# Performance work log

Hardware: AMD Instinct MI355X
Metric: run time of the kernel (lower is better)

## Reference

```python
import jax, jax.numpy as jnp
import numpy as np

B, S, D, H, W = 4, 9, 256, 32, 32
RATIO = 2
NH = 16
DK = D // NH            # 16 (module recomputes d_k = d_in // n_head)
HP, WP = H // RATIO, W // RATIO
QL = H * W              # 1024 query tokens
KL = S * HP * WP        # 2304 key/value tokens


def setup_inputs() -> dict:
    key = jax.random.key(0)
    ks = jax.random.split(key, 8)
    s = 0.02
    return {
        "x": jax.random.normal(ks[0], (B, S, D, H, W), jnp.float32),
        "conv_w": jax.random.normal(ks[1], (D, D, RATIO, RATIO), jnp.float32) * s,
        "conv_b": jnp.zeros((D,), jnp.float32),
        "gn_g": jnp.ones((D,), jnp.float32),
        "gn_b": jnp.zeros((D,), jnp.float32),
        "wq": jax.random.normal(ks[2], (D, NH * DK), jnp.float32) * s,
        "bq": jnp.zeros((NH * DK,), jnp.float32),
        "wkv": jax.random.normal(ks[3], (D, 2 * NH * DK), jnp.float32) * s,
        "bkv": jnp.zeros((2 * NH * DK,), jnp.float32),
        "pos_bias": jax.random.normal(ks[4], (NH, QL, KL), jnp.float32) * s,
        "proj_w": jax.random.normal(ks[5], (D, D), jnp.float32) * s,
        "proj_b": jnp.zeros((D,), jnp.float32),
    }


def reference(x, conv_w, conv_b, gn_g, gn_b, wq, bq, wkv, bkv, pos_bias, proj_w, proj_b):
    b, s, d, h, w = x.shape
    hp, wp = h // RATIO, w // RATIO

    # query stream: center frame, flattened -> (b, h*w, d)
    v_self = x[:, 4].reshape(b, d, h * w).transpose(0, 2, 1)

    # key/value stream: Conv2d(k=stride=ratio) + GroupNorm(NH groups) over all frames
    vn = x.reshape(b * s, d, h, w)
    vn = jax.lax.conv_general_dilated(
        vn, conv_w, window_strides=(RATIO, RATIO), padding="VALID",
        dimension_numbers=("NCHW", "OIHW", "NCHW"))
    vn = vn + conv_b[None, :, None, None]
    g = vn.reshape(b * s, NH, d // NH, hp, wp)
    mu = g.mean(axis=(2, 3, 4), keepdims=True)
    var = g.var(axis=(2, 3, 4), keepdims=True)
    g = (g - mu) * jax.lax.rsqrt(var + 1e-5)
    vn = g.reshape(b * s, d, hp, wp) * gn_g[None, :, None, None] + gn_b[None, :, None, None]
    # (b, s*hp*wp, d)
    vn = vn.reshape(b, s, d, hp, wp).transpose(0, 1, 3, 4, 2).reshape(b, s * hp * wp, d)

    # projections
    q = (v_self @ wq + bq).reshape(b, h * w, NH, DK)            # (b, Q, H, dk)
    kv = (vn @ wkv + bkv).reshape(b, -1, 2, NH, DK)             # (b, K, 2, H, dk)
    k, v = kv[:, :, 0], kv[:, :, 1]                             # (b, K, H, dk)

    # cross-attention with learned positional bias added to QK^T
    dots = jnp.einsum("bqhd,bkhd->hbqk", q, k) * (DK ** -0.5)
    dots = dots + pos_bias[:, None]                             # (H, b, Q, K)
    attn = jax.nn.softmax(dots, axis=-1)
    out = jnp.einsum("hbqk,bkhd->bqhd", attn, v)                # (b, Q, H, dk)
    out = out.reshape(b, h, w, NH * DK)                         # (n c) head-major
    out = out @ proj_w + proj_b                                 # (b, h, w, d)

    # SpatialVit: 'b h w c -> b c h w'
    return out.transpose(0, 3, 1, 2)
```

## Files before the change

### kernel.cpp

```cpp
#include <hip/hip_runtime.h>

#define NBATCH 4
#define NSEQ   9
#define ND     256
#define NHEAD  16
#define NDKv   16
#define NQ     1024
#define NKL    2304
#define NKLH   1152
#define NSAMP  36

constexpr long OFF_CONV = 0;
constexpr long OFF_VN   = 2359296;
constexpr long OFF_WT   = 3538944;
constexpr long OFF_Q    = 4718592;
constexpr long OFF_K    = 5242880;
constexpr long OFF_VT   = 6422528;
constexpr long OFF_AO   = 0;
constexpr long OFF_PN   = 1048576;
constexpr long OFF_PL   = 3145728;

using bf16x8 = __attribute__((ext_vector_type(8))) short;
using f32x4  = __attribute__((ext_vector_type(4))) float;

__device__ __forceinline__ float bf2f(unsigned short h) {
    unsigned int u = ((unsigned int)h) << 16;
    float f; __builtin_memcpy(&f, &u, 4); return f;
}
__device__ __forceinline__ unsigned short f2bf(float f) {
    unsigned int u; __builtin_memcpy(&u, &f, 4);
    u += 0x7fffu + ((u >> 16) & 1u);
    return (unsigned short)(u >> 16);
}
template<bool BF> __device__ __forceinline__ float ld1(const void* p, long i) {
    if constexpr (BF) return bf2f(((const unsigned short*)p)[i]);
    else return ((const float*)p)[i];
}
template<bool BF> __device__ __forceinline__ float4 ld4(const void* p, long i) {
    if constexpr (BF) { ushort4 v = *(const ushort4*)((const unsigned short*)p + i);
                        return make_float4(bf2f(v.x), bf2f(v.y), bf2f(v.z), bf2f(v.w)); }
    else return *(const float4*)((const float*)p + i);
}
template<bool BF> __device__ __forceinline__ void st1(void* p, long i, float v) {
    if constexpr (BF) ((unsigned short*)p)[i] = f2bf(v);
    else ((float*)p)[i] = v;
}
__device__ __forceinline__ bool detect_bf16(const void* gn_g) {
    return (*(const unsigned int*)gn_g) != 0x3F800000u;
}

template<bool BF>
__device__ void conv_body(const void* __restrict__ x, const void* __restrict__ cw,
                          const void* __restrict__ cb, float* __restrict__ ws) {
    __shared__ short lA[64 * 40];
    __shared__ short lB[128 * 40];
    const int tid  = threadIdx.x;
    const int n    = blockIdx.x;
    const int pq   = blockIdx.y;
    const int och  = blockIdx.z;
    const int wave = tid >> 6, lane = tid & 63;
    const int col  = lane & 15, quad = lane >> 4;

    f32x4 acc[4][2];
    #pragma unroll
    for (int mt = 0; mt < 4; ++mt)
        #pragma unroll
        for (int nt = 0; nt < 2; ++nt) acc[mt][nt] = {0.f, 0.f, 0.f, 0.f};

    const int icl  = tid >> 5;
    const int t5   = tid & 31;
    const int ihl  = t5 >> 2;
    const int iwg  = (t5 & 3) * 8;
    const int k0x  = icl * 4 + (ihl & 1) * 2;
    const int posx = (ihl >> 1) * 16 + (iwg >> 1);
    const long xrow = ((long)n * ND * 32 + (long)(pq * 8 + ihl)) * 32 + iwg;

    const int ocw = tid >> 3;
    const int kkw = (tid & 7) * 4;

    for (int kc = 0; kc < 32; ++kc) {
        __syncthreads();
        {
            const long xa = xrow + (long)(kc * 8 + icl) * 1024;
            float4 v0 = ld4<BF>(x, xa);
            float4 v1 = ld4<BF>(x, xa + 4);
            unsigned short us[8] = {f2bf(v0.x), f2bf(v0.y), f2bf(v0.z), f2bf(v0.w),
                                    f2bf(v1.x), f2bf(v1.y), f2bf(v1.z), f2bf(v1.w)};
            #pragma unroll
            for (int o = 0; o < 4; ++o)
                *(ushort2*)&lA[(posx + o) * 40 + k0x] = make_ushort2(us[2*o], us[2*o+1]);
        }
        #pragma unroll
        for (int j = 0; j < 4; ++j) {
            const int oc = ocw + j * 32;
            float4 wv = ld4<BF>(cw, (long)(och * 128 + oc) * 1024 + kc * 32 + kkw);
            unsigned int lo = (unsigned int)f2bf(wv.x) | ((unsigned int)f2bf(wv.y) << 16);
            unsigned int hi = (unsigned int)f2bf(wv.z) | ((unsigned int)f2bf(wv.w) << 16);
            *(uint2*)&lB[oc * 40 + kkw] = make_uint2(lo, hi);
        }
        __syncthreads();
        bf16x8 af[4];
        #pragma unroll
        for (int mt = 0; mt < 4; ++mt)
            af[mt] = *(const bf16x8*)&lA[(mt * 16 + col) * 40 + quad * 8];
        #pragma unroll
        for (int nt = 0; nt < 2; ++nt) {
            bf16x8 bfg = *(const bf16x8*)&lB[((wave * 2 + nt) * 16 + col) * 40 + quad * 8];
            #pragma unroll
            for (int mt = 0; mt < 4; ++mt)
                acc[mt][nt] = __builtin_amdgcn_mfma_f32_16x16x32_bf16(af[mt], bfg, acc[mt][nt], 0, 0, 0);
        }
    }

    float* co = ws + OFF_CONV + (long)n * 65536;
    #pragma unroll
    for (int nt = 0; nt < 2; ++nt) {
        const int oc = och * 128 + (wave * 2 + nt) * 16 + col;
        const float cbv = ld1<BF>(cb, oc);
        #pragma unroll
        for (int mt = 0; mt < 4; ++mt)
            #pragma unroll
            for (int r = 0; r < 4; ++r) {
                const int pos = pq * 64 + mt * 16 + quad * 4 + r;
                co[(long)pos * 256 + oc] = acc[mt][nt][r] + cbv;
            }
    }
}
__global__ void __launch_bounds__(256)
conv_k(const void* x, const void* cw, const void* cb, const void* gg, float* ws) {
    if (detect_bf16(gg)) conv_body<true>(x, cw, cb, ws);
    else                 conv_body<false>(x, cw, cb, ws);
}

template<bool BF>
__device__ void gn_body(const void* __restrict__ gn_g, const void* __restrict__ gn_b,
                        float* __restrict__ ws) {
    const int t = threadIdx.x;
    const int n = blockIdx.x;
    const int g = blockIdx.y;
    const float* row = ws + OFF_CONV + ((long)n * 256 + t) * 256 + g * 16;

    float v[16]; float s1 = 0.f, s2 = 0.f;
    #pragma unroll
    for (int q4 = 0; q4 < 4; ++q4) {
        float4 a = *(const float4*)(row + q4 * 4);
        v[q4*4+0] = a.x; v[q4*4+1] = a.y; v[q4*4+2] = a.z; v[q4*4+3] = a.w;
        s1 += (a.x + a.y) + (a.z + a.w);
        s2 += (a.x*a.x + a.y*a.y) + (a.z*a.z + a.w*a.w);
    }
    __shared__ float r1[4], r2[4];
    #pragma unroll
    for (int off = 32; off > 0; off >>= 1) {
        s1 += __shfl_down(s1, off, 64);
        s2 += __shfl_down(s2, off, 64);
    }
    if ((t & 63) == 0) { r1[t >> 6] = s1; r2[t >> 6] = s2; }
    __syncthreads();
    const float ts1 = r1[0] + r1[1] + r1[2] + r1[3];
    const float ts2 = r2[0] + r2[1] + r2[2] + r2[3];
    const float mean = ts1 * (1.0f / 4096.0f);
    const float var  = ts2 * (1.0f / 4096.0f) - mean * mean;
    const float inv  = rsqrtf(var + 1e-5f);

    const int b = n / NSEQ, s = n % NSEQ;
    float o[16];
    #pragma unroll
    for (int cl = 0; cl < 16; ++cl) {
        float gg = ld1<BF>(gn_g, g * 16 + cl);
        float bb = ld1<BF>(gn_b, g * 16 + cl);
        o[cl] = (v[cl] - mean) * inv * gg + bb;
    }
    unsigned short* dst = (unsigned short*)(ws + OFF_VN)
                          + ((long)b * NKL + s * 256 + t) * ND + g * 16;
    bf16x8 w0, w1;
    #pragma unroll
    for (int cl = 0; cl < 8; ++cl) {
        w0[cl] = (short)f2bf(o[cl]);
        w1[cl] = (short)f2bf(o[cl + 8]);
    }
    *(bf16x8*)dst       = w0;
    *(bf16x8*)(dst + 8) = w1;
}
__global__ void gn_k(const void* gg, const void* gb, float* ws) {
    if (detect_bf16(gg)) gn_body<true>(gg, gb, ws);
    else                 gn_body<false>(gg, gb, ws);
}

template<bool BF>
__device__ void tw_body(const void* __restrict__ wkv, float* __restrict__ ws) {
    __shared__ float tile[16][17];
    const int t = threadIdx.x;
    const int oc0 = blockIdx.x * 16;
    const int r = t >> 4, c = t & 15;
    unsigned short* wt = (unsigned short*)(ws + OFF_WT);
    for (int k0 = 0; k0 < ND; k0 += 16) {
        const float v = ld1<BF>(wkv, (long)(k0 + r) * 512 + oc0 + c);
        __syncthreads();
        tile[r][c] = v;
        __syncthreads();
        wt[(long)(oc0 + r) * ND + k0 + c] = f2bf(tile[c][r]);
    }
}
__global__ void __launch_bounds__(256)
tw_k(const void* wkv, const void* gg, float* ws) {
    if (detect_bf16(gg)) tw_body<true>(wkv, ws);
    else                 tw_body<false>(wkv, ws);
}

template<bool BF>
__device__ void q_body(const void* __restrict__ x, const void* __restrict__ wq,
                       const void* __restrict__ bq, float* __restrict__ ws) {
    const int lane = threadIdx.x;
    const int mb = blockIdx.x;
    const int ob = blockIdx.y;
    const int b  = mb >> 6;
    const int q0 = (mb & 63) * 16;
    const int oc = ob * 64 + lane;

    float acc[16];
    const float bqv = ld1<BF>(bq, oc);
    #pragma unroll
    for (int i = 0; i < 16; ++i) acc[i] = bqv;

    const long xoff = ((long)(b * NSEQ + 4) * ND) * NQ;
    for (int d = 0; d < ND; ++d) {
        const float wv = ld1<BF>(wq, (long)d * 256 + oc);
        const long vb = xoff + (long)d * NQ + q0;
        float4 a0 = ld4<BF>(x, vb + 0);
        float4 a1 = ld4<BF>(x, vb + 4);
        float4 a2 = ld4<BF>(x, vb + 8);
        float4 a3 = ld4<BF>(x, vb + 12);
        acc[0]  += a0.x * wv; acc[1]  += a0.y * wv; acc[2]  += a0.z * wv; acc[3]  += a0.w * wv;
        acc[4]  += a1.x * wv; acc[5]  += a1.y * wv; acc[6]  += a1.z * wv; acc[7]  += a1.w * wv;
        acc[8]  += a2.x * wv; acc[9]  += a2.y * wv; acc[10] += a2.z * wv; acc[11] += a2.w * wv;
        acc[12] += a3.x * wv; acc[13] += a3.y * wv; acc[14] += a3.z * wv; acc[15] += a3.w * wv;
    }
    const int h = oc >> 4, dk = oc & 15;
    unsigned short* qb = (unsigned short*)(ws + OFF_Q);
    #pragma unroll
    for (int i = 0; i < 16; ++i)
        qb[(((long)b * NHEAD + h) * NQ + q0 + i) * NDKv + dk] = f2bf(acc[i]);
}
__global__ void __launch_bounds__(64, 4)
q_k(const void* x, const void* wq, const void* bq, const void* gg, float* ws) {
    if (detect_bf16(gg)) q_body<true>(x, wq, bq, ws);
    else                 q_body<false>(x, wq, bq, ws);
}

template<bool BF>
__device__ void kv_body(const void* __restrict__ bkv, float* __restrict__ ws) {
    __shared__ short lA[64 * 32];
    __shared__ short lB[128 * 32];
    const int tid = threadIdx.x;
    const int b   = blockIdx.x / 36;
    const int t0  = (blockIdx.x % 36) * 64;
    const int ob  = blockIdx.y;
    const int wave = tid >> 6, lane = tid & 63;
    const int col = lane & 15, quad = lane >> 4;

    const unsigned short* vnb = (const unsigned short*)(ws + OFF_VN) + ((long)b * NKL + t0) * ND;
    const unsigned short* wtb = (const unsigned short*)(ws + OFF_WT) + (long)ob * 128 * ND;

    const int rS = tid >> 2;
    const int sS = (tid & 3) * 8;

    f32x4 acc[4][2];
    #pragma unroll
    for (int mt = 0; mt < 4; ++mt)
        #pragma unroll
        for (int nt = 0; nt < 2; ++nt) acc[mt][nt] = {0.f, 0.f, 0.f, 0.f};

    for (int kc = 0; kc < 8; ++kc) {
        __syncthreads();
        *(bf16x8*)&lA[rS * 32 + sS] =
            *(const bf16x8*)(vnb + (long)rS * ND + kc * 32 + sS);
        *(bf16x8*)&lB[rS * 32 + sS] =
            *(const bf16x8*)(wtb + (long)rS * ND + kc * 32 + sS);
        *(bf16x8*)&lB[(64 + rS) * 32 + sS] =
            *(const bf16x8*)(wtb + (long)(64 + rS) * ND + kc * 32 + sS);
        __syncthreads();
        bf16x8 af[4];
        #pragma unroll
        for (int mt = 0; mt < 4; ++mt)
            af[mt] = *(const bf16x8*)&lA[(mt * 16 + col) * 32 + quad * 8];
        #pragma unroll
        for (int nt = 0; nt < 2; ++nt) {
            bf16x8 bfg = *(const bf16x8*)&lB[((wave * 2 + nt) * 16 + col) * 32 + quad * 8];
            #pragma unroll
            for (int mt = 0; mt < 4; ++mt)
                acc[mt][nt] = __builtin_amdgcn_mfma_f32_16x16x32_bf16(af[mt], bfg, acc[mt][nt], 0, 0, 0);
        }
    }

    const bool isv = (ob >= 2);
    unsigned short* k16  = (unsigned short*)(ws + OFF_K);
    unsigned short* vt16 = (unsigned short*)(ws + OFF_VT);
    #pragma unroll
    for (int nt = 0; nt < 2; ++nt) {
        const int ocl = (wave * 2 + nt) * 16 + col;
        const int oc  = ob * 128 + ocl;
        const float bv = ld1<BF>(bkv, oc);
        const int oc2 = oc & 255, h = oc2 >> 4, dk = oc2 & 15;
        if (!isv) {
            #pragma unroll
            for (int mt = 0; mt < 4; ++mt)
                #pragma unroll
                for (int r = 0; r < 4; ++r) {
                    const int tok = t0 + mt * 16 + quad * 4 + r;
                    k16[((long)(b * NHEAD + h) * NKL + tok) * NDKv + dk] = f2bf(acc[mt][nt][r] + bv);
                }
        } else {
            #pragma unroll
            for (int mt = 0; mt < 4; ++mt) {
                const int tok = t0 + mt * 16 + quad * 4;
                ushort4 pk;
                pk.x = f2bf(acc[mt][nt][0] + bv);
                pk.y = f2bf(acc[mt][nt][1] + bv);
                pk.z = f2bf(acc[mt][nt][2] + bv);
                pk.w = f2bf(acc[mt][nt][3] + bv);
                *(ushort4*)&vt16[((long)(b * NHEAD + h) * 16 + dk) * NKL + tok] = pk;
            }
        }
    }
}
__global__ void __launch_bounds__(256)
kv_k(const void* bkv, const void* gg, float* ws) {
    if (detect_bf16(gg)) kv_body<true>(bkv, ws);
    else                 kv_body<false>(bkv, ws);
}

template<bool BF>
__device__ void attn_body(const void* __restrict__ pos_bias, float* __restrict__ ws) {
    __shared__ short lds[4 * 16 * 40];
    const int tid  = threadIdx.x;
    const int b    = tid >> 6;
    const int lane = tid & 63;
    const int qt   = blockIdx.x;
    const int h    = blockIdx.y;
    const int half = blockIdx.z;
    const int t0   = half * NKLH;
    const int bh = b * NHEAD + h;
    const int col  = lane & 15;
    const int quad = lane >> 4;
    short* myl = &lds[b * 640];

    const unsigned short* Qb = (const unsigned short*)(ws + OFF_Q);
    const unsigned short* Kb = (const unsigned short*)(ws + OFF_K);
    const unsigned short* Vt = (const unsigned short*)(ws + OFF_VT);

    bf16x8 qfrag = {0,0,0,0,0,0,0,0};
    if (quad < 2)
        qfrag = *(const bf16x8*)(Qb + (((long)bh * NQ + qt * 16 + col) * 16 + quad * 8));

    const unsigned short* Krows = Kb + ((long)bh * NKL + t0) * 16 + (long)col * 16 + (quad & 1) * 8;
    const unsigned short* Vrow  = Vt + ((long)bh * 16 + col) * NKL + t0 + quad * 8;
    const long pbase = ((long)h * NQ + qt * 16 + col) * NKL + t0 + quad * 4;

    f32x4 oacc = {0.f, 0.f, 0.f, 0.f};
    const f32x4 zc = {0.f, 0.f, 0.f, 0.f};
    float lsum = 0.f;

    auto do_chunk = [&](bf16x8 ck0, bf16x8 ck1, bf16x8 cv, float4 cb0, float4 cb1) {
        f32x4 s0 = __builtin_amdgcn_mfma_f32_16x16x32_bf16(ck0, qfrag, zc, 0, 0, 0);
        f32x4 s1 = __builtin_amdgcn_mfma_f32_16x16x32_bf16(ck1, qfrag, zc, 0, 0, 0);
        float p0 = __expf(s0[0] * 0.25f + cb0.x);
        float p1 = __expf(s0[1] * 0.25f + cb0.y);
        float p2 = __expf(s0[2] * 0.25f + cb0.z);
        float p3 = __expf(s0[3] * 0.25f + cb0.w);
        float r0 = __expf(s1[0] * 0.25f + cb1.x);
        float r1 = __expf(s1[1] * 0.25f + cb1.y);
        float r2 = __expf(s1[2] * 0.25f + cb1.z);
        float r3 = __expf(s1[3] * 0.25f + cb1.w);
        lsum += ((p0 + p1) + (p2 + p3)) + ((r0 + r1) + (r2 + r3));
        unsigned int lo0 = (unsigned int)f2bf(p0) | ((unsigned int)f2bf(p1) << 16);
        unsigned int hi0 = (unsigned int)f2bf(p2) | ((unsigned int)f2bf(p3) << 16);
        unsigned int lo1 = (unsigned int)f2bf(r0) | ((unsigned int)f2bf(r1) << 16);
        unsigned int hi1 = (unsigned int)f2bf(r2) | ((unsigned int)f2bf(r3) << 16);
        *(uint2*)(&myl[col * 40 + quad * 4])      = make_uint2(lo0, hi0);
        *(uint2*)(&myl[col * 40 + 16 + quad * 4]) = make_uint2(lo1, hi1);
        bf16x8 pfrag = *(const bf16x8*)(&myl[col * 40 + quad * 8]);
        oacc = __builtin_amdgcn_mfma_f32_16x16x32_bf16(pfrag, cv, oacc, 0, 0, 0);
    };

    bf16x8 kf0 = *(const bf16x8*)(Krows);
    bf16x8 kf1 = *(const bf16x8*)(Krows + 16L * 16);
    bf16x8 vf  = *(const bf16x8*)(Vrow);
    float4 pbA0 = ld4<BF>(pos_bias, pbase);
    float4 pbA1 = ld4<BF>(pos_bias, pbase + 16);
    float4 pbB0 = ld4<BF>(pos_bias, pbase + 32);
    float4 pbB1 = ld4<BF>(pos_bias, pbase + 48);

    for (int kb = 0; kb < NKLH; kb += 64) {
        {
            const bf16x8 ck0 = kf0, ck1 = kf1, cv = vf;
            const float4 cb0 = pbA0, cb1 = pbA1;
            const int nk = kb + 32;
            kf0 = *(const bf16x8*)(Krows + (long)nk * 16);
            kf1 = *(const bf16x8*)(Krows + (long)(nk + 16) * 16);
            vf  = *(const bf16x8*)(Vrow + nk);
            const int pk = (kb + 64 < NKLH) ? kb + 64 : 0;
            pbA0 = ld4<BF>(pos_bias, pbase + pk);
            pbA1 = ld4<BF>(pos_bias, pbase + pk + 16);
            do_chunk(ck0, ck1, cv, cb0, cb1);
        }
        {
            const bf16x8 ck0 = kf0, ck1 = kf1, cv = vf;
            const float4 cb0 = pbB0, cb1 = pbB1;
            const int nk = (kb + 64 < NKLH) ? kb + 64 : 0;
            kf0 = *(const bf16x8*)(Krows + (long)nk * 16);
            kf1 = *(const bf16x8*)(Krows + (long)(nk + 16) * 16);
            vf  = *(const bf16x8*)(Vrow + nk);
            const int pk = (kb + 96 < NKLH) ? kb + 96 : 0;
            pbB0 = ld4<BF>(pos_bias, pbase + pk);
            pbB1 = ld4<BF>(pos_bias, pbase + pk + 16);
            do_chunk(ck0, ck1, cv, cb0, cb1);
        }
    }

    lsum += __shfl_xor(lsum, 16, 64);
    lsum += __shfl_xor(lsum, 32, 64);

    float* pn = ws + OFF_PN + ((((long)half * NBATCH + b) * NHEAD + h) * NQ + qt * 16) * 16;
    #pragma unroll
    for (int r = 0; r < 4; ++r)
        pn[(long)(quad * 4 + r) * 16 + col] = oacc[r];
    if (quad == 0) {
        float* pl = ws + OFF_PL + (((long)half * NBATCH + b) * NHEAD + h) * NQ + qt * 16;
        pl[col] = lsum;
    }
}
__global__ void __launch_bounds__(256, 8)
attn_k(const void* pos_bias, const void* gg, float* ws) {
    if (detect_bf16(gg)) attn_body<true>(pos_bias, ws);
    else                 attn_body<false>(pos_bias, ws);
}

__global__ void __launch_bounds__(256)
comb_k(float* __restrict__ ws) {
    const int idx = blockIdx.x * 256 + threadIdx.x;
    const int b   = idx >> 18;
    const int rem = idx & 262143;
    const int q   = rem >> 8;
    const int c   = rem & 255;
    const int h   = c >> 4, dv = c & 15;
    const float* pn = ws + OFF_PN;
    const float* pl = ws + OFF_PL;
    const long base0 = (((long)b * NHEAD + h) * NQ + q);
    const long base1 = ((((long)NBATCH + b) * NHEAD + h) * NQ + q);
    const float n = pn[base0 * 16 + dv] + pn[base1 * 16 + dv];
    const float l = pl[base0] + pl[base1];
    ws[OFF_AO + idx] = n / l;
}

template<bool BF>
__device__ void proj_body(const void* __restrict__ pw, const void* __restrict__ pbias,
                          const float* __restrict__ ws, void* __restrict__ out) {
    const int lane = threadIdx.x;
    const int bp = blockIdx.x;
    const int cbk = blockIdx.y;
    const int b = bp >> 4;
    const int p = (bp & 15) * 64 + lane;
    const int c0 = cbk * 16;

    const float* ao = ws + OFF_AO + ((long)b * NQ + p) * ND;
    float acc[16];
    #pragma unroll
    for (int i = 0; i < 16; ++i) acc[i] = ld1<BF>(pbias, c0 + i);

    for (int j = 0; j < ND; j += 4) {
        const float4 av = *(const float4*)(ao + j);
        #pragma unroll
        for (int jj = 0; jj < 4; ++jj) {
            const float a = (jj == 0) ? av.x : (jj == 1) ? av.y : (jj == 2) ? av.z : av.w;
            #pragma unroll
            for (int i = 0; i < 16; ++i) {
                const float w = ld1<BF>(pw, (long)(j + jj) * ND + c0 + i);
                acc[i] += a * w;
            }
        }
    }
    #pragma unroll
    for (int i = 0; i < 16; ++i)
        st1<BF>(out, ((long)b * ND + c0 + i) * NQ + p, acc[i]);
}
__global__ void __launch_bounds__(64, 4)
proj_k(const void* pw, const void* pbias, const void* gg, const float* ws, void* out) {
    if (detect_bf16(gg)) proj_body<true>(pw, pbias, ws, out);
    else                 proj_body<false>(pw, pbias, ws, out);
}

extern "C" void kernel_launch(void* const* d_in, const int* in_sizes, int n_in,
                              void* d_out, int out_size, void* d_ws, size_t ws_size,
                              hipStream_t stream) {
    (void)in_sizes; (void)n_in; (void)out_size; (void)ws_size;
    const void* x   = d_in[0];
    const void* cw  = d_in[1];
    const void* cb  = d_in[2];
    const void* gg  = d_in[3];
    const void* gb  = d_in[4];
    const void* wq  = d_in[5];
    const void* bq  = d_in[6];
    const void* wkv = d_in[7];
    const void* bkv = d_in[8];
    const void* pb  = d_in[9];
    const void* pw  = d_in[10];
    const void* pbb = d_in[11];
    float* ws = (float*)d_ws;

    conv_k   <<<dim3(36, 4, 2), 256, 0, stream>>>(x, cw, cb, gg, ws);
    gn_k     <<<dim3(36, 16),   256, 0, stream>>>(gg, gb, ws);
    tw_k     <<<dim3(32),       256, 0, stream>>>(wkv, gg, ws);
    q_k      <<<dim3(256, 4),    64, 0, stream>>>(x, wq, bq, gg, ws);
    kv_k     <<<dim3(144, 4),   256, 0, stream>>>(bkv, gg, ws);
    attn_k   <<<dim3(64, 16, 2), 256, 0, stream>>>(pb, gg, ws);
    comb_k   <<<dim3(4096),     256, 0, stream>>>(ws);
    proj_k   <<<dim3(64, 16),    64, 0, stream>>>(pw, pbb, gg, ws, d_out);
}
```

Baseline: 517.1 us.

## Stage fp32 pos_bias tiles through swizzled double-buffered LDS in attention

In the fp32 path, the attention kernel now loads the positional-bias tile cooperatively: each thread fetches contiguous float4 segments of a 16x128 slab into XOR-swizzled, double-buffered shared memory, then reads it per chunk. This replaces per-lane strided global bias loads with coalesced loads and prefetches the next slab during compute. The cost is a block-wide barrier per slab, about 16KB of extra LDS, and the launch bound occupancy hint lowered from 8 to 7. The bf16 path is unchanged.

```diff
diff --git a/kernel.cpp b/kernel.cpp
--- a/kernel.cpp
+++ b/kernel.cpp
@@ -331,7 +331,8 @@
 
 template<bool BF>
 __device__ void attn_body(const void* __restrict__ pos_bias, float* __restrict__ ws) {
-    __shared__ short lds[4 * 16 * 40];
+    __shared__ short plds[4 * 16 * 40];
+    __shared__ float biasl[2][16 * 128];
     const int tid  = threadIdx.x;
     const int b    = tid >> 6;
     const int lane = tid & 63;
@@ -342,7 +343,7 @@
     const int bh = b * NHEAD + h;
     const int col  = lane & 15;
     const int quad = lane >> 4;
-    short* myl = &lds[b * 640];
+    short* myl = &plds[b * 640];
 
     const unsigned short* Qb = (const unsigned short*)(ws + OFF_Q);
     const unsigned short* Kb = (const unsigned short*)(ws + OFF_K);
@@ -354,7 +355,6 @@
 
     const unsigned short* Krows = Kb + ((long)bh * NKL + t0) * 16 + (long)col * 16 + (quad & 1) * 8;
     const unsigned short* Vrow  = Vt + ((long)bh * 16 + col) * NKL + t0 + quad * 8;
-    const long pbase = ((long)h * NQ + qt * 16 + col) * NKL + t0 + quad * 4;
 
     f32x4 oacc = {0.f, 0.f, 0.f, 0.f};
     const f32x4 zc = {0.f, 0.f, 0.f, 0.f};
@@ -382,38 +382,89 @@
         oacc = __builtin_amdgcn_mfma_f32_16x16x32_bf16(pfrag, cv, oacc, 0, 0, 0);
     };
 
-    bf16x8 kf0 = *(const bf16x8*)(Krows);
-    bf16x8 kf1 = *(const bf16x8*)(Krows + 16L * 16);
-    bf16x8 vf  = *(const bf16x8*)(Vrow);
-    float4 pbA0 = ld4<BF>(pos_bias, pbase);
-    float4 pbA1 = ld4<BF>(pos_bias, pbase + 16);
-    float4 pbB0 = ld4<BF>(pos_bias, pbase + 32);
-    float4 pbB1 = ld4<BF>(pos_bias, pbase + 48);
-
-    for (int kb = 0; kb < NKLH; kb += 64) {
+    if constexpr (BF) {
+        const long pbase = ((long)h * NQ + qt * 16 + col) * NKL + t0 + quad * 4;
+        bf16x8 kf0 = *(const bf16x8*)(Krows);
+        bf16x8 kf1 = *(const bf16x8*)(Krows + 16L * 16);
+        bf16x8 vf  = *(const bf16x8*)(Vrow);
+        float4 pbA0 = ld4<BF>(pos_bias, pbase);
+        float4 pbA1 = ld4<BF>(pos_bias, pbase + 16);
+        float4 pbB0 = ld4<BF>(pos_bias, pbase + 32);
+        float4 pbB1 = ld4<BF>(pos_bias, pbase + 48);
+        for (int kb = 0; kb < NKLH; kb += 64) {
+            {
+                const bf16x8 ck0 = kf0, ck1 = kf1, cv = vf;
+                const float4 cb0 = pbA0, cb1 = pbA1;
+                const int nk = kb + 32;
+                kf0 = *(const bf16x8*)(Krows + (long)nk * 16);
+                kf1 = *(const bf16x8*)(Krows + (long)(nk + 16) * 16);
+                vf  = *(const bf16x8*)(Vrow + nk);
+                const int pk = (kb + 64 < NKLH) ? kb + 64 : 0;
+                pbA0 = ld4<BF>(pos_bias, pbase + pk);
+                pbA1 = ld4<BF>(pos_bias, pbase + pk + 16);
+                do_chunk(ck0, ck1, cv, cb0, cb1);
+            }
+            {
+                const bf16x8 ck0 = kf0, ck1 = kf1, cv = vf;
+                const float4 cb0 = pbB0, cb1 = pbB1;
+                const int nk = (kb + 64 < NKLH) ? kb + 64 : 0;
+                kf0 = *(const bf16x8*)(Krows + (long)nk * 16);
+                kf1 = *(const bf16x8*)(Krows + (long)(nk + 16) * 16);
+                vf  = *(const bf16x8*)(Vrow + nk);
+                const int pk = (kb + 96 < NKLH) ? kb + 96 : 0;
+                pbB0 = ld4<BF>(pos_bias, pbase + pk);
+                pbB1 = ld4<BF>(pos_bias, pbase + pk + 16);
+                do_chunk(ck0, ck1, cv, cb0, cb1);
+            }
+        }
+    } else {
+        const int srow = tid >> 4;
+        const int sseg = tid & 15;
+        const long growbase = ((long)h * NQ + qt * 16 + srow) * NKL + t0;
+        const int swzw_st = (srow & 7) << 2;
+        const int sw0 = (sseg * 4) ^ swzw_st;
+        const int swz_rd = (col & 7) << 2;
+
         {
-            const bf16x8 ck0 = kf0, ck1 = kf1, cv = vf;
-            const float4 cb0 = pbA0, cb1 = pbA1;
-            const int nk = kb + 32;
-            kf0 = *(const bf16x8*)(Krows + (long)nk * 16);
-            kf1 = *(const bf16x8*)(Krows + (long)(nk + 16) * 16);
-            vf  = *(const bf16x8*)(Vrow + nk);
-            const int pk = (kb + 64 < NKLH) ? kb + 64 : 0;
-            pbA0 = ld4<BF>(pos_bias, pbase + pk);
-            pbA1 = ld4<BF>(pos_bias, pbase + pk + 16);
-            do_chunk(ck0, ck1, cv, cb0, cb1);
-        }
-        {
-            const bf16x8 ck0 = kf0, ck1 = kf1, cv = vf;
-            const float4 cb0 = pbB0, cb1 = pbB1;
-            const int nk = (kb + 64 < NKLH) ? kb + 64 : 0;
-            kf0 = *(const bf16x8*)(Krows + (long)nk * 16);
-            kf1 = *(const bf16x8*)(Krows + (long)(nk + 16) * 16);
-            vf  = *(const bf16x8*)(Vrow + nk);
-            const int pk = (kb + 96 < NKLH) ? kb + 96 : 0;
-            pbB0 = ld4<BF>(pos_bias, pbase + pk);
-            pbB1 = ld4<BF>(pos_bias, pbase + pk + 16);
-            do_chunk(ck0, ck1, cv, cb0, cb1);
+            float4 bA = ld4<false>(pos_bias, growbase + sseg * 4);
+            float4 bB = ld4<false>(pos_bias, growbase + sseg * 4 + 64);
+            float* dst = &biasl[0][srow * 128];
+            *(float4*)&dst[sw0]      = bA;
+            *(float4*)&dst[sw0 + 64] = bB;
+        }
+        __syncthreads();
+
+        bf16x8 kf0 = *(const bf16x8*)(Krows);
+        bf16x8 kf1 = *(const bf16x8*)(Krows + 16L * 16);
+        bf16x8 vf  = *(const bf16x8*)(Vrow);
+
+        for (int ci = 0; ci < 9; ++ci) {
+            float4 bA, bB;
+            if (ci < 8) {
+                const long g = growbase + (ci + 1) * 128 + sseg * 4;
+                bA = ld4<false>(pos_bias, g);
+                bB = ld4<false>(pos_bias, g + 64);
+            }
+            const float* bb = &biasl[ci & 1][col * 128];
+            #pragma unroll
+            for (int sub = 0; sub < 4; ++sub) {
+                const int kb = ci * 128 + sub * 32;
+                const bf16x8 ck0 = kf0, ck1 = kf1, cv = vf;
+                const int nk = (kb + 32 < NKLH) ? kb + 32 : 0;
+                kf0 = *(const bf16x8*)(Krows + (long)nk * 16);
+                kf1 = *(const bf16x8*)(Krows + (long)(nk + 16) * 16);
+                vf  = *(const bf16x8*)(Vrow + nk);
+                const int kl = sub * 32 + quad * 4;
+                float4 cb0 = *(const float4*)&bb[kl ^ swz_rd];
+                float4 cb1 = *(const float4*)&bb[(kl + 16) ^ swz_rd];
+                do_chunk(ck0, ck1, cv, cb0, cb1);
+            }
+            if (ci < 8) {
+                float* dst = &biasl[(ci + 1) & 1][srow * 128];
+                *(float4*)&dst[sw0]      = bA;
+                *(float4*)&dst[sw0 + 64] = bB;
+                __syncthreads();
+            }
         }
     }
 
@@ -429,7 +480,7 @@
         pl[col] = lsum;
     }
 }
-__global__ void __launch_bounds__(256, 8)
+__global__ void __launch_bounds__(256, 7)
 attn_k(const void* pos_bias, const void* gg, float* ws) {
     if (detect_bf16(gg)) attn_body<true>(pos_bias, ws);
     else                 attn_body<false>(pos_bias, ws);
```

Measured after the change: 471.0 us. -8.9%, faster.
